# Kernel optimization log

Measured on AMD Instinct MI355X. Metric: run time of the kernel, lower is better.

Reference implementation:

```python
import jax, jax.numpy as jnp
import numpy as np

B, N, D = 2, 2048, 1024
H = 16
DH = D // H

def setup_inputs() -> dict:
    key = jax.random.key(0)
    ks = jax.random.split(key, 9)
    s = 1.0 / np.sqrt(D)
    return {
        "x": jax.random.normal(ks[0], (B, N, D), dtype=jnp.float32),
        "Wq": jax.random.uniform(ks[1], (D, D), jnp.float32, -s, s),
        "bq": jax.random.uniform(ks[2], (D,), jnp.float32, -s, s),
        "Wk": jax.random.uniform(ks[3], (D, D), jnp.float32, -s, s),
        "bk": jax.random.uniform(ks[4], (D,), jnp.float32, -s, s),
        "Wv": jax.random.uniform(ks[5], (D, D), jnp.float32, -s, s),
        "bv": jax.random.uniform(ks[6], (D,), jnp.float32, -s, s),
        "Wo": jax.random.uniform(ks[7], (D, D), jnp.float32, -s, s),
        "bo": jax.random.uniform(ks[8], (D,), jnp.float32, -s, s),
    }

def reference(x, Wq, bq, Wk, bk, Wv, bv, Wo, bo):
    # torch Linear: y = x @ W.T + b
    scale = 1.0 / np.sqrt(DH)
    q = (x @ Wq.T + bq).reshape(B, N, H, DH).transpose(0, 2, 1, 3)  # [B,H,N,DH]
    k = (x @ Wk.T + bk).reshape(B, N, H, DH).transpose(0, 2, 1, 3)
    v = (x @ Wv.T + bv).reshape(B, N, H, DH).transpose(0, 2, 1, 3)
    scores = jnp.einsum('bhnd,bhmd->bhnm', q, k) * scale  # [B,H,N,N]
    attn = jax.nn.softmax(scores, axis=-1)
    out = jnp.einsum('bhnm,bhmd->bhnd', attn, v)  # [B,H,N,DH]
    out = out.transpose(0, 2, 1, 3).reshape(B, N, D)
    return out @ Wo.T + bo
```

## Files before the change

kernel.cpp:

```cpp
#include <hip/hip_runtime.h>
#include <hip/hip_bf16.h>

#define B_  2
#define N_  2048
#define D_  1024
#define H_  16
#define DH_ 64
#define BN_ (B_*N_)

typedef __attribute__((ext_vector_type(8))) short short8;
typedef __attribute__((ext_vector_type(4))) float f32x4;
typedef __attribute__((ext_vector_type(16))) float f32x16;
typedef __attribute__((ext_vector_type(4))) unsigned int uint4v;

typedef __attribute__((address_space(3))) unsigned int lds_u32_t;
typedef const __attribute__((address_space(1))) unsigned int glb_u32_t;

__device__ __forceinline__ void async_load16(const unsigned short* g, unsigned short* l) {
    __builtin_amdgcn_global_load_lds((glb_u32_t*)g, (lds_u32_t*)l, 16, 0, 0);
}

__device__ __forceinline__ unsigned short f2bf(float f) {
    __hip_bfloat16 h = __float2bfloat16(f);
    return *reinterpret_cast<unsigned short*>(&h);
}

__device__ __forceinline__ unsigned int pkbf(float a, float b) {
    unsigned int ua = __float_as_uint(a) + 0x8000u;
    unsigned int ub = __float_as_uint(b) + 0x8000u;
    return __builtin_amdgcn_perm(ub, ua, 0x07060302);
}

#if __has_builtin(__builtin_amdgcn_exp2f)
#define EXP2(x) __builtin_amdgcn_exp2f(x)
#else
#define EXP2(x) exp2f(x)
#endif

#define QSCL 0.1803368801111204f

__global__ __launch_bounds__(256) void cast_kernel(
    const float* __restrict__ x,  const float* __restrict__ wq,
    const float* __restrict__ wk, const float* __restrict__ wv,
    const float* __restrict__ wo,
    unsigned short* __restrict__ xb,  unsigned short* __restrict__ wqb,
    unsigned short* __restrict__ wkb, unsigned short* __restrict__ wvb,
    unsigned short* __restrict__ wob)
{
    const size_t NX = (size_t)BN_ * D_;
    const size_t NW = (size_t)D_ * D_;
    size_t i = ((size_t)blockIdx.x * 256 + threadIdx.x) * 4;
    const float* src; unsigned short* dst; size_t off;
    if (i < NX) { src = x; dst = xb; off = i; }
    else {
        size_t j = (i - NX) >> 20;
        off = (i - NX) & (NW - 1);
        src = (j == 0) ? wq : (j == 1) ? wk : (j == 2) ? wv : wo;
        dst = (j == 0) ? wqb : (j == 1) ? wkb : (j == 2) ? wvb : wob;
    }
    float4 v = *(const float4*)(src + off);
    ushort4 o;
    o.x = f2bf(v.x); o.y = f2bf(v.y); o.z = f2bf(v.z); o.w = f2bf(v.w);
    *(ushort4*)(dst + off) = o;
}

template<int OUT_MODE>
__device__ __forceinline__ void gemm_body(
    unsigned short* __restrict__ As, unsigned short* __restrict__ Bs,
    const unsigned short* __restrict__ A, const unsigned short* __restrict__ W,
    const float* __restrict__ bias, void* __restrict__ Cout, int bx, int by)
{
    constexpr int K = D_;
    const int tid  = threadIdx.x;
    const int lane = tid & 63;
    const int wave = tid >> 6;
    const int wm = wave & 1, wn = wave >> 1;
    const int l15 = lane & 15, quad = lane >> 4;

    f32x4 acc[4][4] = {};
    const int row0 = by * 128, col0 = bx * 128;

    const int srow = lane >> 3;
    const int scb  = lane & 7;

    for (int k0 = 0; k0 < K; k0 += 64) {
        __syncthreads();
#pragma unroll
        for (int cc = 0; cc < 4; ++cc) {
            int c  = wave * 4 + cc;
            int lr = c * 8 + srow;
            int gcol = k0 + ((scb ^ (lr & 7)) * 8);
            async_load16(A + (size_t)(row0 + lr) * K + gcol, As + c * 512);
            async_load16(W + (size_t)(col0 + lr) * K + gcol, Bs + c * 512);
        }
        __syncthreads();

#pragma unroll
        for (int kf = 0; kf < 2; ++kf) {
            const int swz = ((kf * 4 + quad) ^ (l15 & 7)) * 8;
            short8 af[4], bf[4];
#pragma unroll
            for (int mi = 0; mi < 4; mi++)
                af[mi] = *(const short8*)(&As[(wm * 64 + mi * 16 + l15) * 64 + swz]);
#pragma unroll
            for (int ni = 0; ni < 4; ni++)
                bf[ni] = *(const short8*)(&Bs[(wn * 64 + ni * 16 + l15) * 64 + swz]);
#pragma unroll
            for (int mi = 0; mi < 4; mi++)
#pragma unroll
                for (int ni = 0; ni < 4; ni++)
                    acc[mi][ni] = __builtin_amdgcn_mfma_f32_16x16x32_bf16(
                        af[mi], bf[ni], acc[mi][ni], 0, 0, 0);
        }
    }

#pragma unroll
    for (int ni = 0; ni < 4; ni++) {
        int col = col0 + wn * 64 + ni * 16 + l15;
        float bv = bias[col];
#pragma unroll
        for (int mi = 0; mi < 4; mi++) {
            int row = row0 + wm * 64 + mi * 16 + quad * 4;
            if (OUT_MODE == 2) {
                ushort4 pk;
                pk.x = f2bf(acc[mi][ni][0] + bv);
                pk.y = f2bf(acc[mi][ni][1] + bv);
                pk.z = f2bf(acc[mi][ni][2] + bv);
                pk.w = f2bf(acc[mi][ni][3] + bv);
                *(ushort4*)((unsigned short*)Cout + (size_t)col * BN_ + row) = pk;
            } else {
#pragma unroll
                for (int r = 0; r < 4; r++) {
                    float v = acc[mi][ni][r] + bv;
                    if (OUT_MODE == 3) v *= QSCL;
                    if (OUT_MODE == 0)
                        ((float*)Cout)[(size_t)(row + r) * D_ + col] = v;
                    else
                        ((unsigned short*)Cout)[(size_t)(row + r) * D_ + col] = f2bf(v);
                }
            }
        }
    }
}

__global__ __launch_bounds__(256) void qkv_gemm(
    const unsigned short* __restrict__ xb,
    const unsigned short* __restrict__ wqb, const unsigned short* __restrict__ wkb,
    const unsigned short* __restrict__ wvb,
    const float* __restrict__ bq, const float* __restrict__ bk, const float* __restrict__ bv,
    unsigned short* __restrict__ q, unsigned short* __restrict__ k, unsigned short* __restrict__ vt)
{
    __shared__ __align__(16) unsigned short As[128 * 64];
    __shared__ __align__(16) unsigned short Bs[128 * 64];
    if (blockIdx.z == 0)
        gemm_body<3>(As, Bs, xb, wqb, bq, q,  blockIdx.x, blockIdx.y);
    else if (blockIdx.z == 1)
        gemm_body<1>(As, Bs, xb, wkb, bk, k,  blockIdx.x, blockIdx.y);
    else
        gemm_body<2>(As, Bs, xb, wvb, bv, vt, blockIdx.x, blockIdx.y);
}

__global__ __launch_bounds__(256) void out_gemm(
    const unsigned short* __restrict__ attn, const unsigned short* __restrict__ wob,
    const float* __restrict__ bo, float* __restrict__ out)
{
    __shared__ __align__(16) unsigned short As[128 * 64];
    __shared__ __align__(16) unsigned short Bs[128 * 64];
    gemm_body<0>(As, Bs, attn, wob, bo, out, blockIdx.x, blockIdx.y);
}

__global__ __launch_bounds__(256) void attn_kernel(
    const unsigned short* __restrict__ q, const unsigned short* __restrict__ k,
    const unsigned short* __restrict__ vt, unsigned short* __restrict__ o)
{
    __shared__ __align__(16) unsigned short Ks[2][64 * 64];
    __shared__ __align__(16) unsigned short Vs[2][64 * 64];

    const int tid = threadIdx.x;
    const int lane = tid & 63, wave = tid >> 6;
    const int l31 = lane & 31, kq = lane >> 5;
    const int bh = blockIdx.x;
    const int qt = blockIdx.y;
    const int b = bh >> 4, h = bh & 15;

    const unsigned short* qb = q  + (size_t)b * N_ * D_ + h * DH_;
    const unsigned short* kb = k  + (size_t)b * N_ * D_ + h * DH_;
    const unsigned short* vb = vt + (size_t)h * DH_ * BN_ + (size_t)b * N_;

    const int qrow0 = qt * 128 + wave * 32;

    short8 qf[4];
#pragma unroll
    for (int s = 0; s < 4; s++)
        qf[s] = *(const short8*)(qb + (size_t)(qrow0 + l31) * D_ + s * 16 + kq * 8);

    f32x16 oacc[2] = {};
    float lsum = 0.f;

    const int srow = lane >> 3, scb = lane & 7;

    auto stage = [&](int bi, int kv0) {
#pragma unroll
        for (int cc = 0; cc < 2; ++cc) {
            int c  = wave * 2 + cc;
            int lr = c * 8 + srow;
            int swz8 = (scb ^ (lr & 7)) * 8;
            async_load16(kb + (size_t)(kv0 + lr) * D_ + swz8, (unsigned short*)Ks[bi] + c * 512);
            async_load16(vb + (size_t)lr * BN_ + kv0 + swz8,  (unsigned short*)Vs[bi] + c * 512);
        }
    };

    stage(0, 0);

    const int NIT = N_ / 64;
    for (int it = 0; it < NIT; ++it) {
        const int cur = it & 1;
        __syncthreads();
        if (it + 1 < NIT) stage(cur ^ 1, (it + 1) * 64);

        const unsigned short* Kc = Ks[cur];
        const unsigned short* Vc = Vs[cur];

        f32x16 st[2] = {};
#pragma unroll
        for (int s = 0; s < 4; s++) {
#pragma unroll
            for (int mb = 0; mb < 2; mb++) {
                short8 kfr = *(const short8*)((const char*)Kc +
                    (mb * 32 + l31) * 128 + (((2 * s + kq) ^ (l31 & 7)) * 16));
                st[mb] = __builtin_amdgcn_mfma_f32_32x32x16_bf16(
                    kfr, qf[s], st[mb], 0, 0, 0);
            }
        }

#pragma unroll
        for (int mb = 0; mb < 2; mb++) {
            unsigned int pk[8];
#pragma unroll
            for (int g = 0; g < 4; g++) {
                float p0 = EXP2(st[mb][g * 4 + 0]);
                float p1 = EXP2(st[mb][g * 4 + 1]);
                float p2 = EXP2(st[mb][g * 4 + 2]);
                float p3 = EXP2(st[mb][g * 4 + 3]);
                lsum += (p0 + p1) + (p2 + p3);
                pk[2 * g + 0] = pkbf(p0, p1);
                pk[2 * g + 1] = pkbf(p2, p3);
            }
#pragma unroll
            for (int s = 0; s < 2; s++) {
                uint4v fu;
                fu[0] = pk[4 * s + 0]; fu[1] = pk[4 * s + 1];
                fu[2] = pk[4 * s + 2]; fu[3] = pk[4 * s + 3];
                short8 pf = __builtin_bit_cast(short8, fu);
                const int blkA = 4 * mb + 2 * s;
#pragma unroll
                for (int nb = 0; nb < 2; nb++) {
                    const char* vrow = (const char*)Vc + (nb * 32 + l31) * 128;
                    uint2 vlo = *(const uint2*)(vrow + ((blkA       ^ (l31 & 7)) * 16) + kq * 8);
                    uint2 vhi = *(const uint2*)(vrow + (((blkA + 1) ^ (l31 & 7)) * 16) + kq * 8);
                    uint4v vu; vu[0] = vlo.x; vu[1] = vlo.y; vu[2] = vhi.x; vu[3] = vhi.y;
                    short8 vf = __builtin_bit_cast(short8, vu);
                    oacc[nb] = __builtin_amdgcn_mfma_f32_32x32x16_bf16(
                        pf, vf, oacc[nb], 0, 0, 0);
                }
            }
        }
    }

    lsum += __shfl_xor(lsum, 32);
    __syncthreads();
    float* Lt = (float*)&Ks[0][0] + wave * 32;
    if (kq == 0) Lt[l31] = lsum;
    asm volatile("s_waitcnt lgkmcnt(0)" ::: "memory");

#pragma unroll
    for (int g = 0; g < 4; g++)
#pragma unroll
        for (int rr = 0; rr < 4; rr++) {
            int reg = g * 4 + rr;
            float inv = 1.f / Lt[rr + 8 * g + 4 * kq];
            int row = qrow0 + rr + 8 * g + 4 * kq;
            size_t base = ((size_t)b * N_ + row) * D_ + h * DH_;
#pragma unroll
            for (int nb = 0; nb < 2; nb++)
                o[base + nb * 32 + l31] = f2bf(oacc[nb][reg] * inv);
        }
}

extern "C" void kernel_launch(void* const* d_in, const int* in_sizes, int n_in,
                              void* d_out, int out_size, void* d_ws, size_t ws_size,
                              hipStream_t stream)
{
    const float* x  = (const float*)d_in[0];
    const float* Wq = (const float*)d_in[1];
    const float* bq = (const float*)d_in[2];
    const float* Wk = (const float*)d_in[3];
    const float* bk = (const float*)d_in[4];
    const float* Wv = (const float*)d_in[5];
    const float* bv = (const float*)d_in[6];
    const float* Wo = (const float*)d_in[7];
    const float* bo = (const float*)d_in[8];
    float* out = (float*)d_out;

    char* ws = (char*)d_ws;
    unsigned short* xb  = (unsigned short*)(ws + 0);
    unsigned short* wqb = (unsigned short*)(ws + 8388608);
    unsigned short* wkb = (unsigned short*)(ws + 10485760);
    unsigned short* wvb = (unsigned short*)(ws + 12582912);
    unsigned short* wob = (unsigned short*)(ws + 14680064);
    unsigned short* qd  = (unsigned short*)(ws + 16777216);
    unsigned short* kd  = (unsigned short*)(ws + 25165824);
    unsigned short* vtd = (unsigned short*)(ws + 33554432);
    unsigned short* ad  = (unsigned short*)(ws + 41943040);

    cast_kernel<<<8192, 256, 0, stream>>>(x, Wq, Wk, Wv, Wo, xb, wqb, wkb, wvb, wob);
    qkv_gemm<<<dim3(8, 32, 3), 256, 0, stream>>>(xb, wqb, wkb, wvb, bq, bk, bv, qd, kd, vtd);
    attn_kernel<<<dim3(32, 16), 256, 0, stream>>>(qd, kd, vtd, ad);
    out_gemm<<<dim3(8, 32), 256, 0, stream>>>(ad, wob, bo, out);
}
```

Baseline: 208.1 us.

## Split attention over KV halves with fp32 partials and a combine kernel

New measurement: 219.0 us. 5.3% more time.

```diff
diff --git a/kernel.cpp b/kernel.cpp
--- a/kernel.cpp
+++ b/kernel.cpp
@@ -169,6 +169,147 @@
     gemm_body<0>(As, Bs, attn, wob, bo, out, blockIdx.x, blockIdx.y);
 }
 
+__global__ __launch_bounds__(256) void attn_split(
+    const unsigned short* __restrict__ q, const unsigned short* __restrict__ k,
+    const unsigned short* __restrict__ vt,
+    float* __restrict__ opart, float* __restrict__ lspart)
+{
+    __shared__ __align__(16) unsigned short Ks[2][64 * 64];
+    __shared__ __align__(16) unsigned short Vs[2][64 * 64];
+
+    const int tid = threadIdx.x;
+    const int lane = tid & 63, wave = tid >> 6;
+    const int l31 = lane & 31, kq = lane >> 5;
+    const int bh = blockIdx.x;
+    const int qt = blockIdx.y;
+    const int z  = blockIdx.z;
+    const int b = bh >> 4, h = bh & 15;
+
+    const unsigned short* qb = q  + (size_t)b * N_ * D_ + h * DH_;
+    const unsigned short* kb = k  + (size_t)b * N_ * D_ + h * DH_;
+    const unsigned short* vb = vt + (size_t)h * DH_ * BN_ + (size_t)b * N_;
+
+    const int qrow0 = qt * 128 + wave * 32;
+    const int kvbase = z * (N_ / 2);
+
+    short8 qf[4];
+#pragma unroll
+    for (int s = 0; s < 4; s++)
+        qf[s] = *(const short8*)(qb + (size_t)(qrow0 + l31) * D_ + s * 16 + kq * 8);
+
+    f32x16 oacc[2] = {};
+    float lsum = 0.f;
+
+    const int srow = lane >> 3, scb = lane & 7;
+
+    auto stage = [&](int bi, int kv0) {
+#pragma unroll
+        for (int cc = 0; cc < 2; ++cc) {
+            int c  = wave * 2 + cc;
+            int lr = c * 8 + srow;
+            int swz8 = (scb ^ (lr & 7)) * 8;
+            async_load16(kb + (size_t)(kv0 + lr) * D_ + swz8, (unsigned short*)Ks[bi] + c * 512);
+            async_load16(vb + (size_t)lr * BN_ + kv0 + swz8,  (unsigned short*)Vs[bi] + c * 512);
+        }
+    };
+
+    stage(0, kvbase);
+
+    const int NIT = (N_ / 2) / 64;
+    for (int it = 0; it < NIT; ++it) {
+        const int cur = it & 1;
+        __syncthreads();
+        if (it + 1 < NIT) stage(cur ^ 1, kvbase + (it + 1) * 64);
+
+        const unsigned short* Kc = Ks[cur];
+        const unsigned short* Vc = Vs[cur];
+
+        f32x16 st[2] = {};
+#pragma unroll
+        for (int s = 0; s < 4; s++) {
+#pragma unroll
+            for (int mb = 0; mb < 2; mb++) {
+                short8 kfr = *(const short8*)((const char*)Kc +
+                    (mb * 32 + l31) * 128 + (((2 * s + kq) ^ (l31 & 7)) * 16));
+                st[mb] = __builtin_amdgcn_mfma_f32_32x32x16_bf16(
+                    kfr, qf[s], st[mb], 0, 0, 0);
+            }
+        }
+
+#pragma unroll
+        for (int mb = 0; mb < 2; mb++) {
+            unsigned int pk[8];
+#pragma unroll
+            for (int g = 0; g < 4; g++) {
+                float p0 = EXP2(st[mb][g * 4 + 0]);
+                float p1 = EXP2(st[mb][g * 4 + 1]);
+                float p2 = EXP2(st[mb][g * 4 + 2]);
+                float p3 = EXP2(st[mb][g * 4 + 3]);
+                lsum += (p0 + p1) + (p2 + p3);
+                pk[2 * g + 0] = pkbf(p0, p1);
+                pk[2 * g + 1] = pkbf(p2, p3);
+            }
+#pragma unroll
+            for (int s = 0; s < 2; s++) {
+                uint4v fu;
+                fu[0] = pk[4 * s + 0]; fu[1] = pk[4 * s + 1];
+                fu[2] = pk[4 * s + 2]; fu[3] = pk[4 * s + 3];
+                short8 pf = __builtin_bit_cast(short8, fu);
+                const int blkA = 4 * mb + 2 * s;
+#pragma unroll
+                for (int nb = 0; nb < 2; nb++) {
+                    const char* vrow = (const char*)Vc + (nb * 32 + l31) * 128;
+                    uint2 vlo = *(const uint2*)(vrow + ((blkA       ^ (l31 & 7)) * 16) + kq * 8);
+                    uint2 vhi = *(const uint2*)(vrow + (((blkA + 1) ^ (l31 & 7)) * 16) + kq * 8);
+                    uint4v vu; vu[0] = vlo.x; vu[1] = vlo.y; vu[2] = vhi.x; vu[3] = vhi.y;
+                    short8 vf = __builtin_bit_cast(short8, vu);
+                    oacc[nb] = __builtin_amdgcn_mfma_f32_32x32x16_bf16(
+                        pf, vf, oacc[nb], 0, 0, 0);
+                }
+            }
+        }
+    }
+
+    lsum += __shfl_xor(lsum, 32);
+    if (kq == 0)
+        lspart[(size_t)z * (32 * 2048) + ((size_t)bh << 11) + qrow0 + l31] = lsum;
+
+    float* op = opart + (size_t)z * ((size_t)BN_ * D_);
+#pragma unroll
+    for (int g = 0; g < 4; g++)
+#pragma unroll
+        for (int rr = 0; rr < 4; rr++) {
+            int reg = g * 4 + rr;
+            int row = qrow0 + rr + 8 * g + 4 * kq;
+            size_t base = ((size_t)b * N_ + row) * D_ + h * DH_;
+#pragma unroll
+            for (int nb = 0; nb < 2; nb++)
+                op[base + nb * 32 + l31] = oacc[nb][reg];
+        }
+}
+
+__global__ __launch_bounds__(256) void combine_kernel(
+    const float* __restrict__ opart, const float* __restrict__ lspart,
+    unsigned short* __restrict__ ad)
+{
+    const size_t HALF = (size_t)BN_ * D_;
+    size_t i = ((size_t)blockIdx.x * 256 + threadIdx.x) * 4;
+    int bn = (int)(i >> 10);
+    int h  = (int)((i >> 6) & 15);
+    int b  = bn >> 11, n = bn & 2047;
+    float4 a = *(const float4*)(opart + i);
+    float4 c = *(const float4*)(opart + HALF + i);
+    size_t li = (((size_t)(b * 16 + h)) << 11) + n;
+    float l = lspart[li] + lspart[li + 32 * 2048];
+    float inv = 1.f / l;
+    ushort4 r;
+    r.x = f2bf((a.x + c.x) * inv);
+    r.y = f2bf((a.y + c.y) * inv);
+    r.z = f2bf((a.z + c.z) * inv);
+    r.w = f2bf((a.w + c.w) * inv);
+    *(ushort4*)(ad + i) = r;
+}
+
 __global__ __launch_bounds__(256) void attn_kernel(
     const unsigned short* __restrict__ q, const unsigned short* __restrict__ k,
     const unsigned short* __restrict__ vt, unsigned short* __restrict__ o)
@@ -312,9 +453,17 @@
     unsigned short* kd  = (unsigned short*)(ws + 25165824);
     unsigned short* vtd = (unsigned short*)(ws + 33554432);
     unsigned short* ad  = (unsigned short*)(ws + 41943040);
+    float* opart = (float*)(ws + 50331648);
+    float* lsw   = (float*)(ws + 83886080);
+    const size_t WS_NEED_SPLIT = 84410368;
 
     cast_kernel<<<8192, 256, 0, stream>>>(x, Wq, Wk, Wv, Wo, xb, wqb, wkb, wvb, wob);
     qkv_gemm<<<dim3(8, 32, 3), 256, 0, stream>>>(xb, wqb, wkb, wvb, bq, bk, bv, qd, kd, vtd);
-    attn_kernel<<<dim3(32, 16), 256, 0, stream>>>(qd, kd, vtd, ad);
+    if (ws_size >= WS_NEED_SPLIT) {
+        attn_split<<<dim3(32, 16, 2), 256, 0, stream>>>(qd, kd, vtd, opart, lsw);
+        combine_kernel<<<4096, 256, 0, stream>>>(opart, lsw, ad);
+    } else {
+        attn_kernel<<<dim3(32, 16), 256, 0, stream>>>(qd, kd, vtd, ad);
+    }
     out_gemm<<<dim3(8, 32), 256, 0, stream>>>(ad, wob, bo, out);
 }
```
